# Performance work log

Measured on AMD Instinct MI355X. Metric: run time of the kernel, lower is better.

The kernel has to match this reference:

```python
import jax, jax.numpy as jnp
import numpy as np

N_NODES = 8192
N_EDGES = 65536
MUL = 16          # multiplicity of 0e and 1o irreps
NB = 16           # num_radial_basis
HID = 16          # num_radial_dimension
MAX_RADIUS = 5.0
SQRT3 = float(np.sqrt(3.0))


def soft_unit_step(x):
    # e3nn.math.soft_unit_step: exp(-1/x) for x>0 else 0 (grad-safe where)
    safe = jnp.where(x > 0, x, 1.0)
    return jnp.where(x > 0, jnp.exp(-1.0 / safe), 0.0)


def setup_inputs() -> dict:
    key = jax.random.key(0)
    ks = jax.random.split(key, 12)
    f_in = jax.random.normal(ks[0], (N_NODES, 4 * MUL), jnp.float32)
    edge_vec = jax.random.normal(ks[1], (N_EDGES, 3), jnp.float32) * 1.5
    edge_src = jax.random.randint(ks[2], (N_EDGES,), 0, N_NODES)
    edge_dst = jax.random.randint(ks[3], (N_EDGES,), 0, N_NODES)
    Wq0 = jax.random.normal(ks[4], (MUL, MUL), jnp.float32)
    Wq1 = jax.random.normal(ks[5], (MUL, MUL), jnp.float32)
    Wk1 = jax.random.normal(ks[6], (NB, HID), jnp.float32)
    Wk2 = jax.random.normal(ks[7], (HID, 4 * MUL * MUL), jnp.float32)
    Wv1 = jax.random.normal(ks[8], (NB, HID), jnp.float32)
    Wv2 = jax.random.normal(ks[9], (HID, 4 * MUL * MUL), jnp.float32)
    Wd0 = jax.random.normal(ks[10], (MUL, MUL), jnp.float32)
    Wd1 = jax.random.normal(ks[11], (MUL, MUL), jnp.float32)
    return dict(f_in=f_in, edge_vec=edge_vec, edge_src=edge_src, edge_dst=edge_dst,
                Wq0=Wq0, Wq1=Wq1, Wk1=Wk1, Wk2=Wk2, Wv1=Wv1, Wv2=Wv2, Wd0=Wd0, Wd1=Wd1)


def _forward(f_in, edge_vec, edge_src, edge_dst,
             Wq0, Wq1, Wk1, Wk2, Wv1, Wv2, Wd0, Wd1):
    f0 = f_in[:, :MUL]                         # [N, MUL]    0e scalars
    f1 = f_in[:, MUL:].reshape(-1, MUL, 3)     # [N, MUL, 3] 1o vectors

    r = jnp.linalg.norm(edge_vec, axis=1)      # [E]
    u = edge_vec / r[:, None]
    sh1 = SQRT3 * u                            # Y_1, component norm (|Y1|^2 = 3); Y_0 = 1

    # soft_one_hot_linspace, basis='smooth_finite', cutoff=True, * sqrt(NB)
    values = jnp.linspace(0.0, MAX_RADIUS, NB + 2)
    step = values[1] - values[0]
    diff = (r[:, None] - values[1:-1]) / step
    C = 1.14136 * float(np.exp(2.0))
    rb = (C * soft_unit_step(diff + 1.0) * soft_unit_step(1.0 - diff)) * np.sqrt(NB)

    edge_cut = soft_unit_step(10.0 * (1.0 - r / MAX_RADIUS))  # [E]

    def mlp(x, W1, W2):  # e3nn FullyConnectedNet with fan-in normalization
        h = jax.nn.silu(x @ (W1 / np.sqrt(NB)))
        return h @ (W2 / np.sqrt(HID))

    wk = mlp(rb, Wk1, Wk2).reshape(-1, 4, MUL, MUL)  # per-edge TP weights
    wv = mlp(rb, Wv1, Wv2).reshape(-1, 4, MUL, MUL)

    # h_q: per-irrep linear
    q0 = f0 @ Wq0 / np.sqrt(MUL)
    q1 = jnp.einsum('nic,io->noc', f1, Wq1) / np.sqrt(MUL)

    x0 = f0[edge_src]   # [E, MUL]
    x1 = f1[edge_src]   # [E, MUL, 3]

    def fctp(w):
        # FullyConnectedTensorProduct (16x0e+16x1o) x (0e+1o) -> (16x0e+16x1o)
        # 4 paths: 0x0->0, 1x1->0 (dot/sqrt3), 0x1->1, 1x0->1
        a = 1.0 / np.sqrt(2 * MUL)
        o0 = jnp.einsum('eij,ei->ej', w[:, 0], x0) \
           + jnp.einsum('eij,eic,ec->ej', w[:, 1], x1, sh1) / SQRT3
        o1 = jnp.einsum('eij,ei,ec->ejc', w[:, 2], x0, sh1) \
           + jnp.einsum('eij,eic->ejc', w[:, 3], x1)
        return o0 * a, o1 * a

    k0, k1 = fctp(wk)
    v0, v1 = fctp(wv)

    # dot_product: FCTP(query, key) -> 0e
    ad = 1.0 / np.sqrt(2.0 * MUL * MUL)
    dot = ad * (jnp.einsum('ij,ei,ej->e', Wd0, q0[edge_dst], k0)
                + jnp.einsum('ij,eic,ejc->e', Wd1, q1[edge_dst], k1) / SQRT3)

    exp = edge_cut * jnp.exp(dot)                                   # [E]
    z = jax.ops.segment_sum(exp, edge_dst, num_segments=N_NODES)    # [N]
    z = jnp.where(z == 0.0, 1.0, z)
    alpha = exp / z[edge_dst]
    # alpha.relu().sqrt() with grad-safe sqrt at 0
    s = jnp.where(alpha > 0, jnp.sqrt(jnp.where(alpha > 0, alpha, 1.0)), 0.0)

    f_out0 = jax.ops.segment_sum(s[:, None] * v0, edge_dst, num_segments=N_NODES)
    f_out1 = jax.ops.segment_sum(s[:, None, None] * v1, edge_dst, num_segments=N_NODES)
    return jnp.concatenate([f_out0, f_out1.reshape(-1, MUL * 3)], axis=-1)  # [N, 64]


def reference(f_in, edge_vec, edge_src, edge_dst,
              Wq0, Wq1, Wk1, Wk2, Wv1, Wv2, Wd0, Wd1):
    return _forward(f_in, edge_vec, edge_src, edge_dst,
                    Wq0, Wq1, Wk1, Wk2, Wv1, Wv2, Wd0, Wd1)
```

## Files before the change

### kernel.cpp

```cpp
#include <hip/hip_runtime.h>
#include <hip/hip_bf16.h>

#define N_NODES 8192
#define N_EDGES 65536

#define CNT_OFF  0
#define RP_OFF   8192
#define WF_OFF   16640
#define QD0_OFF  33024
#define QD1_OFF  164096
#define EXP_OFF  557312
#define VH_OFF   622848

typedef _Float16 half8 __attribute__((ext_vector_type(8)));
typedef float f32x4 __attribute__((ext_vector_type(4)));

__device__ __forceinline__ float sus_f(float x) { return x > 0.f ? expf(-1.f / x) : 0.f; }
__device__ __forceinline__ float silu_f(float x) { return x / (1.f + expf(-x)); }

__device__ __forceinline__ half8 vmul(half8 v, _Float16 s) {
    half8 r;
#pragma unroll
    for (int d = 0; d < 8; ++d) r[d] = v[d] * s;
    return r;
}

__global__ __launch_bounds__(256) void k_prep(
    const float* __restrict__ f_in,
    const float* __restrict__ Wq0, const float* __restrict__ Wq1,
    const float* __restrict__ Wd0, const float* __restrict__ Wd1,
    const float* __restrict__ Wk2, const float* __restrict__ Wv2,
    const int* __restrict__ edst,
    half8* __restrict__ wfrag, float* __restrict__ qd0, float* __restrict__ qd1,
    int* __restrict__ cnt) {
    __shared__ float f0s[16][16];
    __shared__ float f1s[16][48];
    __shared__ float t0s[16][16];
    __shared__ float t1s[16][48];
    const int blk = blockIdx.x;
    const int tid = threadIdx.x;

    if (blk < 16) {
        int g = blk * 256 + tid;
        int lane = g & 63, t = (g >> 6) & 7, b = (g >> 9) & 3, kv = g >> 11;
        const float* src = kv ? Wv2 : Wk2;
        int n = lane & 15, quad = lane >> 4;
        const float SC = 0.044194173824159216f;
        half8 out;
#pragma unroll
        for (int d = 0; d < 8; ++d) {
            int k = t * 32 + quad * 8 + d;
            int i = k & 15, h = k >> 4;
            out[d] = (_Float16)(src[h * 1024 + b * 256 + i * 16 + n] * SC);
        }
        wfrag[g] = out;
        return;
    }
    if (blk >= 528) {
        int base = (blk - 528) * 256 + tid;
#pragma unroll
        for (int k = 0; k < 4; ++k) atomicAdd(cnt + edst[base + k * 16384], 1);
        return;
    }
    const int j = tid & 15, ln = tid >> 4;
    const int n = (blk - 16) * 16 + ln;
    f0s[ln][j]         = f_in[n * 64 + j];
    f1s[ln][j * 3 + 0] = f_in[n * 64 + 16 + j * 3 + 0];
    f1s[ln][j * 3 + 1] = f_in[n * 64 + 16 + j * 3 + 1];
    f1s[ln][j * 3 + 2] = f_in[n * 64 + 16 + j * 3 + 2];
    __syncthreads();
    float t0 = 0.f, ta = 0.f, tb = 0.f, tc = 0.f;
#pragma unroll
    for (int p = 0; p < 16; ++p) {
        float wq0 = Wq0[p * 16 + j];
        float wq1 = Wq1[p * 16 + j];
        t0 += f0s[ln][p] * wq0;
        ta += f1s[ln][p * 3 + 0] * wq1;
        tb += f1s[ln][p * 3 + 1] * wq1;
        tc += f1s[ln][p * 3 + 2] * wq1;
    }
    t0s[ln][j] = t0;
    t1s[ln][j * 3 + 0] = ta; t1s[ln][j * 3 + 1] = tb; t1s[ln][j * 3 + 2] = tc;
    __syncthreads();
    float q0a = 0.f, qa = 0.f, qb = 0.f, qc = 0.f;
#pragma unroll
    for (int i = 0; i < 16; ++i) {
        float wd0 = Wd0[i * 16 + j];
        float wd1 = Wd1[i * 16 + j];
        q0a += t0s[ln][i] * wd0;
        qa  += t1s[ln][i * 3 + 0] * wd1;
        qb  += t1s[ln][i * 3 + 1] * wd1;
        qc  += t1s[ln][i * 3 + 2] * wd1;
    }
    const float S0 = 0.011048543456f;
    const float S1 = 0.0063788674817f;
    qd0[n * 16 + j] = q0a * S0;
    qd1[0 * 131072 + n * 16 + j] = qa * S1;
    qd1[1 * 131072 + n * 16 + j] = qb * S1;
    qd1[2 * 131072 + n * 16 + j] = qc * S1;
}

__global__ __launch_bounds__(1024) void k_scan(int* __restrict__ cnt, int* __restrict__ rowptr) {
    __shared__ int wsum[16];
    __shared__ int woff[16];
    const int t = threadIdx.x;
    const int lane = t & 63, wv = t >> 6;
    const int base = t * 8;
    int v[8]; int s = 0;
    int4 p0 = ((const int4*)cnt)[t * 2];
    int4 p1 = ((const int4*)cnt)[t * 2 + 1];
    v[0] = p0.x; v[1] = p0.y; v[2] = p0.z; v[3] = p0.w;
    v[4] = p1.x; v[5] = p1.y; v[6] = p1.z; v[7] = p1.w;
#pragma unroll
    for (int i = 0; i < 8; ++i) s += v[i];
    int own = s;
#pragma unroll
    for (int off = 1; off < 64; off <<= 1) {
        int u = __shfl_up(s, off);
        if (lane >= off) s += u;
    }
    if (lane == 63) wsum[wv] = s;
    __syncthreads();
    if (wv == 0 && lane < 16) {
        int u = wsum[lane];
        int sc = u;
#pragma unroll
        for (int off = 1; off < 16; off <<= 1) {
            int x = __shfl_up(sc, off);
            if (lane >= off) sc += x;
        }
        woff[lane] = sc - u;
    }
    __syncthreads();
    int run = woff[wv] + (s - own);
#pragma unroll
    for (int i = 0; i < 8; ++i) { rowptr[base + i] = run; cnt[base + i] = run; run += v[i]; }
    if (t == 1023) rowptr[8192] = run;
}

__global__ __launch_bounds__(256) void k_edge(
    const float* __restrict__ f_in, const float* __restrict__ evec,
    const int* __restrict__ esrc, const int* __restrict__ edst,
    const float* __restrict__ Wk1, const float* __restrict__ Wv1,
    const half8* __restrict__ wfrag,
    const float* __restrict__ qd0, const float* __restrict__ qd1,
    int* __restrict__ cursor, float* __restrict__ expbuf, _Float16* __restrict__ vh) {
    __shared__ __align__(16) _Float16 s_x0h[64][24];
    __shared__ __align__(16) _Float16 s_xsh[64][24];
    __shared__ __align__(16) _Float16 s_x1h[3][64][24];
    __shared__ __align__(16) _Float16 s_hkh[64][16];
    __shared__ __align__(16) _Float16 s_hvh[64][16];
    __shared__ __align__(16) _Float16 s_vt[64][72];
    __shared__ float s_rb[64][16];
    __shared__ float s_sh[64][4];
    __shared__ int   s_slot[64];

    const int tid = threadIdx.x;
    const int e0 = blockIdx.x * 64;

    {
        const int el = tid >> 2, q = tid & 3;
        const int e = e0 + el;
        float v0 = evec[e * 3 + 0];
        float v1 = evec[e * 3 + 1];
        float v2 = evec[e * 3 + 2];
        float r = sqrtf(v0 * v0 + v1 * v1 + v2 * v2);
        float rs = r * 3.4f;
#pragma unroll
        for (int bb = 0; bb < 4; ++bb) {
            int b = q * 4 + bb;
            s_rb[el][b] = 33.734292f * sus_f(rs - (float)b) * sus_f((float)(b + 2) - rs);
        }
        if (q == 0) {
            float inv = r > 0.f ? 1.f / r : 0.f;
            const float SQ3 = 1.7320508075688772f;
            s_sh[el][0] = SQ3 * v0 * inv;
            s_sh[el][1] = SQ3 * v1 * inv;
            s_sh[el][2] = SQ3 * v2 * inv;
            s_sh[el][3] = sus_f(10.f - 2.f * r);
        }
    }
    __syncthreads();

    {
        const int j = tid & 15, slot = tid >> 4;
#pragma unroll
        for (int s = 0; s < 4; ++s) {
            const int el = slot * 4 + s;
            const int e = e0 + el;
            float aK = 0.f, aV = 0.f;
#pragma unroll
            for (int b = 0; b < 16; ++b) {
                float rbv = s_rb[el][b];
                aK += rbv * Wk1[b * 16 + j];
                aV += rbv * Wv1[b * 16 + j];
            }
            s_hkh[el][(j & 1) * 8 + (j >> 1)] = (_Float16)silu_f(aK * 0.25f);
            s_hvh[el][(j & 1) * 8 + (j >> 1)] = (_Float16)silu_f(aV * 0.25f);
            const int src = esrc[e];
            float x0 = f_in[src * 64 + j];
            float xa = f_in[src * 64 + 16 + j * 3 + 0];
            float xb = f_in[src * 64 + 16 + j * 3 + 1];
            float xc = f_in[src * 64 + 16 + j * 3 + 2];
            s_x0h[el][j] = (_Float16)x0;
            s_x1h[0][el][j] = (_Float16)xa;
            s_x1h[1][el][j] = (_Float16)xb;
            s_x1h[2][el][j] = (_Float16)xc;
            s_xsh[el][j] = (_Float16)((xa * s_sh[el][0] + xb * s_sh[el][1] + xc * s_sh[el][2])
                                      * 0.57735026919f);
        }
    }
    __syncthreads();

    const int lane = tid & 63;
    const int wv = tid >> 6;
    const int m = lane & 15, quad = lane >> 4;
    const int eb = wv * 16;
    const int eloc = eb + m;
    const int ihalf = quad >> 1;
    const int hh = (quad & 1) * 8;

    half8 X0 = *(const half8*)&s_x0h[eloc][hh];
    half8 XS = *(const half8*)&s_xsh[eloc][hh];
    half8 Xa = *(const half8*)&s_x1h[0][eloc][hh];
    half8 Xb = *(const half8*)&s_x1h[1][eloc][hh];
    half8 Xc = *(const half8*)&s_x1h[2][eloc][hh];
    half8 HK = *(const half8*)&s_hkh[eloc][ihalf * 8];
    half8 HV = *(const half8*)&s_hvh[eloc][ihalf * 8];

    {
        f32x4 o0 = {0.f, 0.f, 0.f, 0.f}, a1 = o0, ax = o0, ay = o0, az = o0;
#pragma unroll
        for (int t = 0; t < 8; ++t) {
            _Float16 hs = HK[t];
            half8 B0 = wfrag[(0 * 8 + t) * 64 + lane];
            half8 B1 = wfrag[(1 * 8 + t) * 64 + lane];
            half8 B2 = wfrag[(2 * 8 + t) * 64 + lane];
            half8 B3 = wfrag[(3 * 8 + t) * 64 + lane];
            half8 A0 = vmul(X0, hs);
            half8 As = vmul(XS, hs);
            half8 Aa = vmul(Xa, hs);
            half8 Ab = vmul(Xb, hs);
            half8 Ac = vmul(Xc, hs);
            o0 = __builtin_amdgcn_mfma_f32_16x16x32_f16(A0, B0, o0, 0, 0, 0);
            o0 = __builtin_amdgcn_mfma_f32_16x16x32_f16(As, B1, o0, 0, 0, 0);
            a1 = __builtin_amdgcn_mfma_f32_16x16x32_f16(A0, B2, a1, 0, 0, 0);
            ax = __builtin_amdgcn_mfma_f32_16x16x32_f16(Aa, B3, ax, 0, 0, 0);
            ay = __builtin_amdgcn_mfma_f32_16x16x32_f16(Ab, B3, ay, 0, 0, 0);
            az = __builtin_amdgcn_mfma_f32_16x16x32_f16(Ac, B3, az, 0, 0, 0);
        }
        const int j = m;
#pragma unroll
        for (int r = 0; r < 4; ++r) {
            const int el = eb + quad * 4 + r;
            const int e = e0 + el;
            const int dst = edst[e];
            float sh0 = s_sh[el][0], sh1 = s_sh[el][1], sh2 = s_sh[el][2];
            float k1x = a1[r] * sh0 + ax[r];
            float k1y = a1[r] * sh1 + ay[r];
            float k1z = a1[r] * sh2 + az[r];
            float dp = qd0[dst * 16 + j] * o0[r]
                     + qd1[0 * 131072 + dst * 16 + j] * k1x
                     + qd1[1 * 131072 + dst * 16 + j] * k1y
                     + qd1[2 * 131072 + dst * 16 + j] * k1z;
            dp += __shfl_xor(dp, 1);
            dp += __shfl_xor(dp, 2);
            dp += __shfl_xor(dp, 4);
            dp += __shfl_xor(dp, 8);
            if (j == 0) {
                float ev = s_sh[el][3] * expf(dp);
                int slot = atomicAdd(cursor + dst, 1);
                s_slot[el] = slot;
                expbuf[slot] = ev;
            }
        }
    }

    {
        f32x4 o0 = {0.f, 0.f, 0.f, 0.f}, a1 = o0, ax = o0, ay = o0, az = o0;
        const half8* wfv = wfrag + 32 * 64;
#pragma unroll
        for (int t = 0; t < 8; ++t) {
            _Float16 hs = HV[t];
            half8 B0 = wfv[(0 * 8 + t) * 64 + lane];
            half8 B1 = wfv[(1 * 8 + t) * 64 + lane];
            half8 B2 = wfv[(2 * 8 + t) * 64 + lane];
            half8 B3 = wfv[(3 * 8 + t) * 64 + lane];
            half8 A0 = vmul(X0, hs);
            half8 As = vmul(XS, hs);
            half8 Aa = vmul(Xa, hs);
            half8 Ab = vmul(Xb, hs);
            half8 Ac = vmul(Xc, hs);
            o0 = __builtin_amdgcn_mfma_f32_16x16x32_f16(A0, B0, o0, 0, 0, 0);
            o0 = __builtin_amdgcn_mfma_f32_16x16x32_f16(As, B1, o0, 0, 0, 0);
            a1 = __builtin_amdgcn_mfma_f32_16x16x32_f16(A0, B2, a1, 0, 0, 0);
            ax = __builtin_amdgcn_mfma_f32_16x16x32_f16(Aa, B3, ax, 0, 0, 0);
            ay = __builtin_amdgcn_mfma_f32_16x16x32_f16(Ab, B3, ay, 0, 0, 0);
            az = __builtin_amdgcn_mfma_f32_16x16x32_f16(Ac, B3, az, 0, 0, 0);
        }
        const int j = m;
#pragma unroll
        for (int r = 0; r < 4; ++r) {
            const int el = eb + quad * 4 + r;
            float sh0 = s_sh[el][0], sh1 = s_sh[el][1], sh2 = s_sh[el][2];
            s_vt[el][j] = (_Float16)o0[r];
            s_vt[el][16 + j * 3 + 0] = (_Float16)(a1[r] * sh0 + ax[r]);
            s_vt[el][16 + j * 3 + 1] = (_Float16)(a1[r] * sh1 + ay[r]);
            s_vt[el][16 + j * 3 + 2] = (_Float16)(a1[r] * sh2 + az[r]);
        }
    }
    __syncthreads();

#pragma unroll
    for (int pass = 0; pass < 2; ++pass) {
        int row = pass * 32 + (tid >> 3);
        int part = tid & 7;
        half8 val = *(const half8*)&s_vt[row][part * 8];
        int slot = s_slot[row];
        *(half8*)(vh + (size_t)slot * 64 + part * 8) = val;
    }
}

__global__ __launch_bounds__(256) void k_out(
    const int* __restrict__ rowptr,
    const float* __restrict__ expbuf, const _Float16* __restrict__ vh,
    float* __restrict__ fout) {
    const int col = threadIdx.x & 63;
    const int n = blockIdx.x * 4 + (threadIdx.x >> 6);
    const int s0 = rowptr[n], s1 = rowptr[n + 1];
    float zs = 0.f;
    for (int p = s0 + col; p < s1; p += 64) zs += expbuf[p];
#pragma unroll
    for (int off = 32; off > 0; off >>= 1) zs += __shfl_xor(zs, off);
    float zinv = zs > 0.f ? 1.f / zs : 0.f;
    float acc = 0.f;
    for (int p = s0; p < s1; ++p) {
        float ev = expbuf[p];
        float s = ev > 0.f ? sqrtf(ev * zinv) : 0.f;
        acc += s * (float)vh[(size_t)p * 64 + col];
    }
    fout[n * 64 + col] = acc;
}

extern "C" void kernel_launch(void* const* d_in, const int* in_sizes, int n_in,
                              void* d_out, int out_size, void* d_ws, size_t ws_size,
                              hipStream_t stream) {
    const float* f_in = (const float*)d_in[0];
    const float* evec = (const float*)d_in[1];
    const int* esrc = (const int*)d_in[2];
    const int* edst = (const int*)d_in[3];
    const float* Wq0 = (const float*)d_in[4];
    const float* Wq1 = (const float*)d_in[5];
    const float* Wk1 = (const float*)d_in[6];
    const float* Wk2 = (const float*)d_in[7];
    const float* Wv1 = (const float*)d_in[8];
    const float* Wv2 = (const float*)d_in[9];
    const float* Wd0 = (const float*)d_in[10];
    const float* Wd1 = (const float*)d_in[11];

    float* ws     = (float*)d_ws;
    int*   cnt    = (int*)(ws + CNT_OFF);
    int*   rowptr = (int*)(ws + RP_OFF);
    half8* wfrag  = (half8*)(ws + WF_OFF);
    float* qd0    = ws + QD0_OFF;
    float* qd1    = ws + QD1_OFF;
    float* expb   = ws + EXP_OFF;
    _Float16* vh  = (_Float16*)(ws + VH_OFF);
    float* fout   = (float*)d_out;

    hipMemsetAsync(cnt, 0, (size_t)8192 * sizeof(int), stream);

    k_prep<<<592, 256, 0, stream>>>(f_in, Wq0, Wq1, Wd0, Wd1, Wk2, Wv2, edst,
                                    wfrag, qd0, qd1, cnt);
    k_scan<<<1, 1024, 0, stream>>>(cnt, rowptr);
    k_edge<<<N_EDGES / 64, 256, 0, stream>>>(f_in, evec, esrc, edst, Wk1, Wv1,
                                             wfrag, qd0, qd1, cnt, expb, vh);
    k_out<<<N_NODES / 4, 256, 0, stream>>>(rowptr, expb, vh, fout);
}
```

Before: 127.1 us.

## Fuse histogram and scan into one prep block; process 128 edges per block

The memset, the global-atomic histogram and the separate scan kernel are replaced by a single block inside k_prep. That block builds the dst histogram in 32 KB of shared memory, scans it and writes rowptr and the cursors, which removes two launches. k_edge now handles 128 edges per block, each wave running two 16-edge MFMA groups that reuse the same weight fragment loads, with s_rb and s_vt sharing one shared-memory arena. The cost is that one block serially reads all 65536 edges while the other prep blocks run, and k_prep now carries 32 KB of LDS, which may lower its occupancy.

```diff
diff --git a/kernel.cpp b/kernel.cpp
--- a/kernel.cpp
+++ b/kernel.cpp
@@ -4,8 +4,8 @@
 #define N_NODES 8192
 #define N_EDGES 65536
 
-#define CNT_OFF  0
-#define RP_OFF   8192
+#define RP_OFF   0
+#define CNT_OFF  8448
 #define WF_OFF   16640
 #define QD0_OFF  33024
 #define QD1_OFF  164096
@@ -32,11 +32,13 @@
     const float* __restrict__ Wk2, const float* __restrict__ Wv2,
     const int* __restrict__ edst,
     half8* __restrict__ wfrag, float* __restrict__ qd0, float* __restrict__ qd1,
-    int* __restrict__ cnt) {
+    int* __restrict__ cnt, int* __restrict__ rowptr) {
+    __shared__ int hist[8192];
     __shared__ float f0s[16][16];
     __shared__ float f1s[16][48];
     __shared__ float t0s[16][16];
     __shared__ float t1s[16][48];
+    __shared__ int wbase_s[4];
     const int blk = blockIdx.x;
     const int tid = threadIdx.x;
 
@@ -56,10 +58,43 @@
         wfrag[g] = out;
         return;
     }
-    if (blk >= 528) {
-        int base = (blk - 528) * 256 + tid;
-#pragma unroll
-        for (int k = 0; k < 4; ++k) atomicAdd(cnt + edst[base + k * 16384], 1);
+    if (blk == 528) {
+#pragma unroll
+        for (int i = 0; i < 32; ++i) hist[tid * 32 + i] = 0;
+        __syncthreads();
+        const int4* e4 = (const int4*)edst;
+        for (int i = 0; i < 64; ++i) {
+            int4 v = e4[i * 256 + tid];
+            atomicAdd(&hist[v.x], 1);
+            atomicAdd(&hist[v.y], 1);
+            atomicAdd(&hist[v.z], 1);
+            atomicAdd(&hist[v.w], 1);
+        }
+        __syncthreads();
+        int s = 0;
+#pragma unroll
+        for (int i = 0; i < 32; ++i) s += hist[tid * 32 + i];
+        int own = s;
+        const int lane = tid & 63, wv = tid >> 6;
+#pragma unroll
+        for (int off = 1; off < 64; off <<= 1) {
+            int u = __shfl_up(s, off);
+            if (lane >= off) s += u;
+        }
+        if (lane == 63) wbase_s[wv] = s;
+        __syncthreads();
+        int wb = 0;
+#pragma unroll
+        for (int w = 0; w < 4; ++w) if (w < wv) wb += wbase_s[w];
+        int run = wb + (s - own);
+#pragma unroll
+        for (int i = 0; i < 32; ++i) {
+            int idx = tid * 32 + i;
+            rowptr[idx] = run;
+            cnt[idx] = run;
+            run += hist[idx];
+        }
+        if (tid == 255) rowptr[8192] = run;
         return;
     }
     const int j = tid & 15, ln = tid >> 4;
@@ -100,44 +135,6 @@
     qd1[2 * 131072 + n * 16 + j] = qc * S1;
 }
 
-__global__ __launch_bounds__(1024) void k_scan(int* __restrict__ cnt, int* __restrict__ rowptr) {
-    __shared__ int wsum[16];
-    __shared__ int woff[16];
-    const int t = threadIdx.x;
-    const int lane = t & 63, wv = t >> 6;
-    const int base = t * 8;
-    int v[8]; int s = 0;
-    int4 p0 = ((const int4*)cnt)[t * 2];
-    int4 p1 = ((const int4*)cnt)[t * 2 + 1];
-    v[0] = p0.x; v[1] = p0.y; v[2] = p0.z; v[3] = p0.w;
-    v[4] = p1.x; v[5] = p1.y; v[6] = p1.z; v[7] = p1.w;
-#pragma unroll
-    for (int i = 0; i < 8; ++i) s += v[i];
-    int own = s;
-#pragma unroll
-    for (int off = 1; off < 64; off <<= 1) {
-        int u = __shfl_up(s, off);
-        if (lane >= off) s += u;
-    }
-    if (lane == 63) wsum[wv] = s;
-    __syncthreads();
-    if (wv == 0 && lane < 16) {
-        int u = wsum[lane];
-        int sc = u;
-#pragma unroll
-        for (int off = 1; off < 16; off <<= 1) {
-            int x = __shfl_up(sc, off);
-            if (lane >= off) sc += x;
-        }
-        woff[lane] = sc - u;
-    }
-    __syncthreads();
-    int run = woff[wv] + (s - own);
-#pragma unroll
-    for (int i = 0; i < 8; ++i) { rowptr[base + i] = run; cnt[base + i] = run; run += v[i]; }
-    if (t == 1023) rowptr[8192] = run;
-}
-
 __global__ __launch_bounds__(256) void k_edge(
     const float* __restrict__ f_in, const float* __restrict__ evec,
     const int* __restrict__ esrc, const int* __restrict__ edst,
@@ -145,21 +142,22 @@
     const half8* __restrict__ wfrag,
     const float* __restrict__ qd0, const float* __restrict__ qd1,
     int* __restrict__ cursor, float* __restrict__ expbuf, _Float16* __restrict__ vh) {
-    __shared__ __align__(16) _Float16 s_x0h[64][24];
-    __shared__ __align__(16) _Float16 s_xsh[64][24];
-    __shared__ __align__(16) _Float16 s_x1h[3][64][24];
-    __shared__ __align__(16) _Float16 s_hkh[64][16];
-    __shared__ __align__(16) _Float16 s_hvh[64][16];
-    __shared__ __align__(16) _Float16 s_vt[64][72];
-    __shared__ float s_rb[64][16];
-    __shared__ float s_sh[64][4];
-    __shared__ int   s_slot[64];
+    __shared__ __align__(16) _Float16 s_x0h[128][16];
+    __shared__ __align__(16) _Float16 s_xsh[128][16];
+    __shared__ __align__(16) _Float16 s_x1h[3][128][16];
+    __shared__ __align__(16) _Float16 s_hkh[128][16];
+    __shared__ __align__(16) _Float16 s_hvh[128][16];
+    __shared__ float s_sh[128][4];
+    __shared__ int   s_slot[128];
+    __shared__ __align__(16) char s_arena[19456];
+    float (*s_rb)[17] = (float(*)[17])s_arena;
+    _Float16 (*s_vt)[76] = (_Float16(*)[76])s_arena;
 
     const int tid = threadIdx.x;
-    const int e0 = blockIdx.x * 64;
+    const int e0 = blockIdx.x * 128;
 
     {
-        const int el = tid >> 2, q = tid & 3;
+        const int el = tid >> 1, q = tid & 1;
         const int e = e0 + el;
         float v0 = evec[e * 3 + 0];
         float v1 = evec[e * 3 + 1];
@@ -167,8 +165,8 @@
         float r = sqrtf(v0 * v0 + v1 * v1 + v2 * v2);
         float rs = r * 3.4f;
 #pragma unroll
-        for (int bb = 0; bb < 4; ++bb) {
-            int b = q * 4 + bb;
+        for (int bb = 0; bb < 8; ++bb) {
+            int b = q * 8 + bb;
             s_rb[el][b] = 33.734292f * sus_f(rs - (float)b) * sus_f((float)(b + 2) - rs);
         }
         if (q == 0) {
@@ -185,8 +183,8 @@
     {
         const int j = tid & 15, slot = tid >> 4;
 #pragma unroll
-        for (int s = 0; s < 4; ++s) {
-            const int el = slot * 4 + s;
+        for (int s = 0; s < 8; ++s) {
+            const int el = slot * 8 + s;
             const int e = e0 + el;
             float aK = 0.f, aV = 0.f;
 #pragma unroll
@@ -215,51 +213,66 @@
     const int lane = tid & 63;
     const int wv = tid >> 6;
     const int m = lane & 15, quad = lane >> 4;
-    const int eb = wv * 16;
-    const int eloc = eb + m;
+    const int ewb = wv * 32;
     const int ihalf = quad >> 1;
     const int hh = (quad & 1) * 8;
 
-    half8 X0 = *(const half8*)&s_x0h[eloc][hh];
-    half8 XS = *(const half8*)&s_xsh[eloc][hh];
-    half8 Xa = *(const half8*)&s_x1h[0][eloc][hh];
-    half8 Xb = *(const half8*)&s_x1h[1][eloc][hh];
-    half8 Xc = *(const half8*)&s_x1h[2][eloc][hh];
-    half8 HK = *(const half8*)&s_hkh[eloc][ihalf * 8];
-    half8 HV = *(const half8*)&s_hvh[eloc][ihalf * 8];
-
+    half8 X0[2], XS[2], Xa[2], Xb[2], Xc[2], HK[2], HV[2];
+#pragma unroll
+    for (int g = 0; g < 2; ++g) {
+        const int elg = ewb + g * 16 + m;
+        X0[g] = *(const half8*)&s_x0h[elg][hh];
+        XS[g] = *(const half8*)&s_xsh[elg][hh];
+        Xa[g] = *(const half8*)&s_x1h[0][elg][hh];
+        Xb[g] = *(const half8*)&s_x1h[1][elg][hh];
+        Xc[g] = *(const half8*)&s_x1h[2][elg][hh];
+        HK[g] = *(const half8*)&s_hkh[elg][ihalf * 8];
+        HV[g] = *(const half8*)&s_hvh[elg][ihalf * 8];
+    }
+
+    f32x4 o0[2], a1[2], ax[2], ay[2], az[2];
+
+#pragma unroll
+    for (int g = 0; g < 2; ++g) {
+        o0[g] = (f32x4){0.f, 0.f, 0.f, 0.f};
+        a1[g] = o0[g]; ax[g] = o0[g]; ay[g] = o0[g]; az[g] = o0[g];
+    }
+#pragma unroll
+    for (int t = 0; t < 8; ++t) {
+        half8 B0 = wfrag[(0 * 8 + t) * 64 + lane];
+        half8 B1 = wfrag[(1 * 8 + t) * 64 + lane];
+        half8 B2 = wfrag[(2 * 8 + t) * 64 + lane];
+        half8 B3 = wfrag[(3 * 8 + t) * 64 + lane];
+#pragma unroll
+        for (int g = 0; g < 2; ++g) {
+            _Float16 hs = HK[g][t];
+            half8 A0 = vmul(X0[g], hs);
+            half8 As = vmul(XS[g], hs);
+            half8 Aa = vmul(Xa[g], hs);
+            half8 Ab = vmul(Xb[g], hs);
+            half8 Ac = vmul(Xc[g], hs);
+            o0[g] = __builtin_amdgcn_mfma_f32_16x16x32_f16(A0, B0, o0[g], 0, 0, 0);
+            o0[g] = __builtin_amdgcn_mfma_f32_16x16x32_f16(As, B1, o0[g], 0, 0, 0);
+            a1[g] = __builtin_amdgcn_mfma_f32_16x16x32_f16(A0, B2, a1[g], 0, 0, 0);
+            ax[g] = __builtin_amdgcn_mfma_f32_16x16x32_f16(Aa, B3, ax[g], 0, 0, 0);
+            ay[g] = __builtin_amdgcn_mfma_f32_16x16x32_f16(Ab, B3, ay[g], 0, 0, 0);
+            az[g] = __builtin_amdgcn_mfma_f32_16x16x32_f16(Ac, B3, az[g], 0, 0, 0);
+        }
+    }
     {
-        f32x4 o0 = {0.f, 0.f, 0.f, 0.f}, a1 = o0, ax = o0, ay = o0, az = o0;
-#pragma unroll
-        for (int t = 0; t < 8; ++t) {
-            _Float16 hs = HK[t];
-            half8 B0 = wfrag[(0 * 8 + t) * 64 + lane];
-            half8 B1 = wfrag[(1 * 8 + t) * 64 + lane];
-            half8 B2 = wfrag[(2 * 8 + t) * 64 + lane];
-            half8 B3 = wfrag[(3 * 8 + t) * 64 + lane];
-            half8 A0 = vmul(X0, hs);
-            half8 As = vmul(XS, hs);
-            half8 Aa = vmul(Xa, hs);
-            half8 Ab = vmul(Xb, hs);
-            half8 Ac = vmul(Xc, hs);
-            o0 = __builtin_amdgcn_mfma_f32_16x16x32_f16(A0, B0, o0, 0, 0, 0);
-            o0 = __builtin_amdgcn_mfma_f32_16x16x32_f16(As, B1, o0, 0, 0, 0);
-            a1 = __builtin_amdgcn_mfma_f32_16x16x32_f16(A0, B2, a1, 0, 0, 0);
-            ax = __builtin_amdgcn_mfma_f32_16x16x32_f16(Aa, B3, ax, 0, 0, 0);
-            ay = __builtin_amdgcn_mfma_f32_16x16x32_f16(Ab, B3, ay, 0, 0, 0);
-            az = __builtin_amdgcn_mfma_f32_16x16x32_f16(Ac, B3, az, 0, 0, 0);
-        }
         const int j = m;
 #pragma unroll
+        for (int g = 0; g < 2; ++g)
+#pragma unroll
         for (int r = 0; r < 4; ++r) {
-            const int el = eb + quad * 4 + r;
+            const int el = ewb + g * 16 + quad * 4 + r;
             const int e = e0 + el;
             const int dst = edst[e];
             float sh0 = s_sh[el][0], sh1 = s_sh[el][1], sh2 = s_sh[el][2];
-            float k1x = a1[r] * sh0 + ax[r];
-            float k1y = a1[r] * sh1 + ay[r];
-            float k1z = a1[r] * sh2 + az[r];
-            float dp = qd0[dst * 16 + j] * o0[r]
+            float k1x = a1[g][r] * sh0 + ax[g][r];
+            float k1y = a1[g][r] * sh1 + ay[g][r];
+            float k1z = a1[g][r] * sh2 + az[g][r];
+            float dp = qd0[dst * 16 + j] * o0[g][r]
                      + qd1[0 * 131072 + dst * 16 + j] * k1x
                      + qd1[1 * 131072 + dst * 16 + j] * k1y
                      + qd1[2 * 131072 + dst * 16 + j] * k1z;
@@ -276,45 +289,54 @@
         }
     }
 
+#pragma unroll
+    for (int g = 0; g < 2; ++g) {
+        o0[g] = (f32x4){0.f, 0.f, 0.f, 0.f};
+        a1[g] = o0[g]; ax[g] = o0[g]; ay[g] = o0[g]; az[g] = o0[g];
+    }
+    const half8* wfv = wfrag + 32 * 64;
+#pragma unroll
+    for (int t = 0; t < 8; ++t) {
+        half8 B0 = wfv[(0 * 8 + t) * 64 + lane];
+        half8 B1 = wfv[(1 * 8 + t) * 64 + lane];
+        half8 B2 = wfv[(2 * 8 + t) * 64 + lane];
+        half8 B3 = wfv[(3 * 8 + t) * 64 + lane];
+#pragma unroll
+        for (int g = 0; g < 2; ++g) {
+            _Float16 hs = HV[g][t];
+            half8 A0 = vmul(X0[g], hs);
+            half8 As = vmul(XS[g], hs);
+            half8 Aa = vmul(Xa[g], hs);
+            half8 Ab = vmul(Xb[g], hs);
+            half8 Ac = vmul(Xc[g], hs);
+            o0[g] = __builtin_amdgcn_mfma_f32_16x16x32_f16(A0, B0, o0[g], 0, 0, 0);
+            o0[g] = __builtin_amdgcn_mfma_f32_16x16x32_f16(As, B1, o0[g], 0, 0, 0);
+            a1[g] = __builtin_amdgcn_mfma_f32_16x16x32_f16(A0, B2, a1[g], 0, 0, 0);
+            ax[g] = __builtin_amdgcn_mfma_f32_16x16x32_f16(Aa, B3, ax[g], 0, 0, 0);
+            ay[g] = __builtin_amdgcn_mfma_f32_16x16x32_f16(Ab, B3, ay[g], 0, 0, 0);
+            az[g] = __builtin_amdgcn_mfma_f32_16x16x32_f16(Ac, B3, az[g], 0, 0, 0);
+        }
+    }
     {
-        f32x4 o0 = {0.f, 0.f, 0.f, 0.f}, a1 = o0, ax = o0, ay = o0, az = o0;
-        const half8* wfv = wfrag + 32 * 64;
-#pragma unroll
-        for (int t = 0; t < 8; ++t) {
-            _Float16 hs = HV[t];
-            half8 B0 = wfv[(0 * 8 + t) * 64 + lane];
-            half8 B1 = wfv[(1 * 8 + t) * 64 + lane];
-            half8 B2 = wfv[(2 * 8 + t) * 64 + lane];
-            half8 B3 = wfv[(3 * 8 + t) * 64 + lane];
-            half8 A0 = vmul(X0, hs);
-            half8 As = vmul(XS, hs);
-            half8 Aa = vmul(Xa, hs);
-            half8 Ab = vmul(Xb, hs);
-            half8 Ac = vmul(Xc, hs);
-            o0 = __builtin_amdgcn_mfma_f32_16x16x32_f16(A0, B0, o0, 0, 0, 0);
-            o0 = __builtin_amdgcn_mfma_f32_16x16x32_f16(As, B1, o0, 0, 0, 0);
-            a1 = __builtin_amdgcn_mfma_f32_16x16x32_f16(A0, B2, a1, 0, 0, 0);
-            ax = __builtin_amdgcn_mfma_f32_16x16x32_f16(Aa, B3, ax, 0, 0, 0);
-            ay = __builtin_amdgcn_mfma_f32_16x16x32_f16(Ab, B3, ay, 0, 0, 0);
-            az = __builtin_amdgcn_mfma_f32_16x16x32_f16(Ac, B3, az, 0, 0, 0);
-        }
         const int j = m;
 #pragma unroll
+        for (int g = 0; g < 2; ++g)
+#pragma unroll
         for (int r = 0; r < 4; ++r) {
-            const int el = eb + quad * 4 + r;
+            const int el = ewb + g * 16 + quad * 4 + r;
             float sh0 = s_sh[el][0], sh1 = s_sh[el][1], sh2 = s_sh[el][2];
-            s_vt[el][j] = (_Float16)o0[r];
-            s_vt[el][16 + j * 3 + 0] = (_Float16)(a1[r] * sh0 + ax[r]);
-            s_vt[el][16 + j * 3 + 1] = (_Float16)(a1[r] * sh1 + ay[r]);
-            s_vt[el][16 + j * 3 + 2] = (_Float16)(a1[r] * sh2 + az[r]);
-        }
-    }
-    __syncthreads();
-
-#pragma unroll
-    for (int pass = 0; pass < 2; ++pass) {
-        int row = pass * 32 + (tid >> 3);
-        int part = tid & 7;
+            s_vt[el][j] = (_Float16)o0[g][r];
+            s_vt[el][16 + j * 3 + 0] = (_Float16)(a1[g][r] * sh0 + ax[g][r]);
+            s_vt[el][16 + j * 3 + 1] = (_Float16)(a1[g][r] * sh1 + ay[g][r]);
+            s_vt[el][16 + j * 3 + 2] = (_Float16)(a1[g][r] * sh2 + az[g][r]);
+        }
+    }
+    __syncthreads();
+
+#pragma unroll
+    for (int pass = 0; pass < 4; ++pass) {
+        int idx = pass * 256 + tid;
+        int row = idx >> 3, part = idx & 7;
         half8 val = *(const half8*)&s_vt[row][part * 8];
         int slot = s_slot[row];
         *(half8*)(vh + (size_t)slot * 64 + part * 8) = val;
@@ -359,8 +381,8 @@
     const float* Wd1 = (const float*)d_in[11];
 
     float* ws     = (float*)d_ws;
+    int*   rowptr = (int*)(ws + RP_OFF);
     int*   cnt    = (int*)(ws + CNT_OFF);
-    int*   rowptr = (int*)(ws + RP_OFF);
     half8* wfrag  = (half8*)(ws + WF_OFF);
     float* qd0    = ws + QD0_OFF;
     float* qd1    = ws + QD1_OFF;
@@ -368,12 +390,9 @@
     _Float16* vh  = (_Float16*)(ws + VH_OFF);
     float* fout   = (float*)d_out;
 
-    hipMemsetAsync(cnt, 0, (size_t)8192 * sizeof(int), stream);
-
-    k_prep<<<592, 256, 0, stream>>>(f_in, Wq0, Wq1, Wd0, Wd1, Wk2, Wv2, edst,
-                                    wfrag, qd0, qd1, cnt);
-    k_scan<<<1, 1024, 0, stream>>>(cnt, rowptr);
-    k_edge<<<N_EDGES / 64, 256, 0, stream>>>(f_in, evec, esrc, edst, Wk1, Wv1,
-                                             wfrag, qd0, qd1, cnt, expb, vh);
+    k_prep<<<529, 256, 0, stream>>>(f_in, Wq0, Wq1, Wd0, Wd1, Wk2, Wv2, edst,
+                                    wfrag, qd0, qd1, cnt, rowptr);
+    k_edge<<<N_EDGES / 128, 256, 0, stream>>>(f_in, evec, esrc, edst, Wk1, Wv1,
+                                              wfrag, qd0, qd1, cnt, expb, vh);
     k_out<<<N_NODES / 4, 256, 0, stream>>>(rowptr, expb, vh, fout);
 }
```

Result: slower. 151.9 us (+19.5%).
